# Kernel optimization log

Hardware: AMD Instinct MI355X
Metric: run time of the kernel (lower is better)

## Reference

```python
import jax, jax.numpy as jnp
import numpy as np

DIM = 1024
NUM_HEADS = 8
HEAD_DIM = 128
MAX_SEQ_LEN = 2048
ATTN_SCALE = 0.12
RMS_EPS = 1.1920929e-07  # torch float32 eps (F.rms_norm default)


def rms_norm(x):
    return x * jax.lax.rsqrt(jnp.mean(jnp.square(x), axis=-1, keepdims=True) + RMS_EPS)


def rope_tables(T):
    # angular_freq: (1/1024)**linspace(0,1,head_dim//4), padded with head_dim//4 zeros -> length head_dim//2
    af = (1.0 / 1024.0) ** np.linspace(0.0, 1.0, HEAD_DIM // 4, dtype=np.float32)
    af = np.concatenate([af, np.zeros(HEAD_DIM // 4, dtype=np.float32)])
    t = np.arange(T, dtype=np.float32)
    theta = np.einsum('i,j->ij', t, af)  # [T, head_dim//2]
    return jnp.asarray(np.cos(theta)), jnp.asarray(np.sin(theta))


def apply_rope(x_BTHD, cos, sin):
    # cos/sin: [T, head_dim//2] -> broadcast [1,T,1,hd//2]
    c = cos[None, :, None, :]
    s = sin[None, :, None, :]
    x1, x2 = jnp.split(x_BTHD, 2, axis=-1)
    y1 = x1 * c + x2 * s
    y2 = -x1 * s + x2 * c
    return jnp.concatenate([y1, y2], axis=-1)


def setup_inputs() -> dict:
    key = jax.random.key(0)
    k1, k2, k3, k4, k5 = jax.random.split(key, 5)
    B, T = 4, 2048
    hdim = NUM_HEADS * HEAD_DIM
    std = 0.5 * DIM ** (-0.5)
    bound = (3.0 ** 0.5) * std
    x = jax.random.normal(k1, (B, T, DIM), dtype=jnp.float32)
    ve = jax.random.normal(k2, (B, T, DIM), dtype=jnp.float32)
    sa_lambdas = jax.random.uniform(k3, (2,), dtype=jnp.float32)
    qkv_w = jax.random.uniform(k4, (3, hdim, DIM), dtype=jnp.float32, minval=-bound, maxval=bound)
    # original inits c_proj to zeros; use small random so the output is non-trivial
    c_proj_weight = jax.random.normal(k5, (DIM, hdim), dtype=jnp.float32) * 0.02
    return {"x": x, "ve": ve, "sa_lambdas": sa_lambdas, "qkv_w": qkv_w,
            "c_proj_weight": c_proj_weight}


def reference(x, ve, sa_lambdas, qkv_w, c_proj_weight):
    B, T, D = x.shape
    H, hd = NUM_HEADS, HEAD_DIM
    Wqkv = qkv_w.reshape(3 * H * hd, D)
    qkv = jnp.einsum('btd,ed->bte', x, Wqkv).reshape(B, T, 3 * H, hd)
    q, k, v = jnp.split(qkv, 3, axis=-2)  # each [B,T,H,hd]
    q, k = rms_norm(q), rms_norm(k)
    cos, sin = rope_tables(T)
    q, k = apply_rope(q, cos, sin), apply_rope(k, cos, sin)
    v = sa_lambdas[0] * v + sa_lambdas[1] * ve.reshape(B, T, H, hd)
    # [B,H,T,T] scores
    attn = jnp.einsum('bqhd,bkhd->bhqk', q, k) * ATTN_SCALE
    causal = jnp.triu(jnp.ones((T, T), dtype=bool), k=1)
    attn = jnp.where(causal[None, None], -jnp.inf, attn)
    attn = jax.nn.softmax(attn, axis=-1)
    y = jnp.einsum('bhqk,bkhd->bqhd', attn, v).reshape(B, T, H * hd)
    return jnp.einsum('bte,de->btd', y, c_proj_weight)
```

## Files before the change

kernel.cpp:

```cpp
#include <hip/hip_runtime.h>

#define DIM 1024
#define NH 8
#define HD 128
#define T_SEQ 2048
#define NTOK 8192
#define QKV_N 3072
#define ATTN_SCALE 0.12f
#define RMS_EPS 1.1920929e-07f

using f32x4  = __attribute__((ext_vector_type(4))) float;
using bf16x8 = __attribute__((ext_vector_type(8))) __bf16;

__device__ __forceinline__ unsigned short f2bf(float f) {
    unsigned int u = __builtin_bit_cast(unsigned int, f);
    u += 0x7fffu + ((u >> 16) & 1u);
    return (unsigned short)(u >> 16);
}
__device__ __forceinline__ float bf2f(unsigned short s) {
    unsigned int u = ((unsigned int)s) << 16;
    return __builtin_bit_cast(float, u);
}
__device__ __forceinline__ unsigned int cvtpk(float lo, float hi) {
    unsigned int r;
    asm("v_cvt_pk_bf16_f32 %0, %1, %2" : "=v"(r) : "v"(lo), "v"(hi));
    return r;
}

__device__ __forceinline__ void gll16(const void* g, void* l) {
    __builtin_amdgcn_global_load_lds(
        (const __attribute__((address_space(1))) unsigned int*)g,
        (__attribute__((address_space(3))) unsigned int*)l, 16, 0, 0);
}

#define VMCNT(n) asm volatile("s_waitcnt vmcnt(" #n ")" ::: "memory")

__global__ __launch_bounds__(256) void prep(const float* __restrict__ x,
                                            const float* __restrict__ qkvw,
                                            const float* __restrict__ cprojw,
                                            unsigned short* __restrict__ xb,
                                            unsigned short* __restrict__ wqb,
                                            unsigned short* __restrict__ cpb,
                                            float2* __restrict__ tab) {
    const int bid = blockIdx.x;
    const int tid = threadIdx.x;
    if (bid < 12288) {
        const float* in;
        unsigned short* out;
        int i;
        if (bid < 8192)        { in = x;      out = xb;  i = bid*256 + tid; }
        else if (bid < 11264)  { in = qkvw;   out = wqb; i = (bid-8192)*256 + tid; }
        else                   { in = cprojw; out = cpb; i = (bid-11264)*256 + tid; }
        float4 f = ((const float4*)in)[i];
        ushort4 o;
        o.x = f2bf(f.x); o.y = f2bf(f.y); o.z = f2bf(f.z); o.w = f2bf(f.w);
        ((ushort4*)out)[i] = o;
    } else {
        int idx = (bid - 12288)*256 + tid;
        int t = idx >> 5, i = idx & 31;
        float th = (float)t * exp2f((float)i * (-10.0f/31.0f));
        float sn, cs;
        sincosf(th, &sn, &cs);
        tab[idx] = make_float2(cs, sn);
    }
}

#define SLOT_A 32768
#define SLOT_SZ 49152

template<int OUTF32>
__global__ __launch_bounds__(512, 1) void gemm256(const unsigned short* __restrict__ A,
                                                  const unsigned short* __restrict__ B,
                                                  void* __restrict__ Cout,
                                                  int M, int N, int K, int nbn) {
    __shared__ __align__(16) char smem[147456];
    const int tid  = threadIdx.x;
    const int lane = tid & 63;
    const int w    = tid >> 6;
    const int wm   = w >> 1, wn = w & 1;
    const int lr   = lane & 15, lg = lane >> 4;
    const int xsw  = (lr & 7) << 3;

    const int chunk = gridDim.x >> 3;
    const int bid2  = (blockIdx.x & 7) * chunk + (blockIdx.x >> 3);
    const int m0 = (bid2 / nbn) * 256;
    const int n0 = (bid2 % nbn) * 128;

    const int rsub = lane >> 3;
    const int csw  = ((lane & 7) ^ rsub) << 3;

    char* s0 = smem;
    char* s1 = smem + SLOT_SZ;
    char* s2 = smem + 2*SLOT_SZ;

    auto stage = [&](int kt, char* slot) {
        const int kb = kt * 64;
        #pragma unroll
        for (int i = 0; i < 4; ++i) {
            int c = w*4 + i;
            gll16(&A[(size_t)(m0 + c*8 + rsub)*K + kb + csw], slot + c*1024);
        }
        #pragma unroll
        for (int i = 0; i < 2; ++i) {
            int c = w*2 + i;
            gll16(&B[(size_t)(n0 + c*8 + rsub)*K + kb + csw], slot + SLOT_A + c*1024);
        }
    };

    f32x4 acc[4][4] = {};
    const int KT = K / 64;

    stage(0, s0);
    stage(1, s1);
    VMCNT(6);
    __builtin_amdgcn_s_barrier();
    __builtin_amdgcn_sched_barrier(0);

    for (int t = 0; t < KT; ++t) {
        if (t + 2 < KT) stage(t + 2, s2);
        const unsigned short* sA = (const unsigned short*)s0;
        const unsigned short* sB = (const unsigned short*)(s0 + SLOT_A);
        bf16x8 bfr[4][2];
        #pragma unroll
        for (int n = 0; n < 4; ++n)
            #pragma unroll
            for (int kk = 0; kk < 2; ++kk)
                bfr[n][kk] = *(const bf16x8*)&sB[(wn*64 + n*16 + lr)*64 + ((kk*32 + lg*8) ^ xsw)];
        #pragma unroll
        for (int m = 0; m < 4; ++m) {
            bf16x8 af[2];
            #pragma unroll
            for (int kk = 0; kk < 2; ++kk)
                af[kk] = *(const bf16x8*)&sA[(wm*64 + m*16 + lr)*64 + ((kk*32 + lg*8) ^ xsw)];
            __builtin_amdgcn_s_setprio(1);
            #pragma unroll
            for (int n = 0; n < 4; ++n)
                #pragma unroll
                for (int kk = 0; kk < 2; ++kk)
                    acc[m][n] = __builtin_amdgcn_mfma_f32_16x16x32_bf16(af[kk], bfr[n][kk], acc[m][n], 0, 0, 0);
            __builtin_amdgcn_s_setprio(0);
        }
        if (t + 2 < KT) { VMCNT(6); }
        else            { VMCNT(0); }
        __builtin_amdgcn_s_barrier();
        __builtin_amdgcn_sched_barrier(0);
        char* tmp = s0; s0 = s1; s1 = s2; s2 = tmp;
    }

    __syncthreads();
    float* sc = (float*)(smem + (size_t)w * 17408);
    #pragma unroll
    for (int m = 0; m < 4; ++m)
        #pragma unroll
        for (int n = 0; n < 4; ++n)
            #pragma unroll
            for (int r = 0; r < 4; ++r)
                sc[(m*16 + lg*4 + r)*68 + n*16 + lr] = acc[m][n][r];

    if (OUTF32) {
        float* C = (float*)Cout;
        #pragma unroll
        for (int rnd = 0; rnd < 16; ++rnd) {
            int g = rnd*64 + lane;
            int row = g >> 4, c4 = (g & 15) * 4;
            float4 v = *(float4*)&sc[row*68 + c4];
            *(float4*)&C[(size_t)(m0 + wm*64 + row)*N + n0 + wn*64 + c4] = v;
        }
    } else {
        unsigned short* C = (unsigned short*)Cout;
        #pragma unroll
        for (int rnd = 0; rnd < 8; ++rnd) {
            int g = rnd*64 + lane;
            int row = g >> 3, c8 = (g & 7) * 8;
            float4 v0 = *(float4*)&sc[row*68 + c8];
            float4 v1 = *(float4*)&sc[row*68 + c8 + 4];
            uint4 o;
            o.x = f2bf(v0.x) | ((unsigned)f2bf(v0.y) << 16);
            o.y = f2bf(v0.z) | ((unsigned)f2bf(v0.w) << 16);
            o.z = f2bf(v1.x) | ((unsigned)f2bf(v1.y) << 16);
            o.w = f2bf(v1.z) | ((unsigned)f2bf(v1.w) << 16);
            *(uint4*)&C[(size_t)(m0 + wm*64 + row)*N + n0 + wn*64 + c8] = o;
        }
    }
}

__global__ __launch_bounds__(256) void qkv_post(const unsigned short* __restrict__ qkv,
                                                const float2* __restrict__ tab,
                                                unsigned short* __restrict__ qO,
                                                unsigned short* __restrict__ kO) {
    int gw   = (blockIdx.x * 256 + threadIdx.x) >> 6;
    int lane = threadIdx.x & 63;
    int h     = gw & 7;
    int token = gw >> 3;
    int t     = token & (T_SEQ-1);
    int b     = token >> 11;

    const unsigned short* base = qkv + (size_t)token * QKV_N + h*HD;
    float q1 = bf2f(base[lane]),        q2 = bf2f(base[lane+64]);
    float k1 = bf2f(base[1024+lane]),   k2 = bf2f(base[1024+lane+64]);

    float sq = q1*q1 + q2*q2;
    float sk = k1*k1 + k2*k2;
    #pragma unroll
    for (int m = 1; m < 64; m <<= 1) {
        sq += __shfl_xor(sq, m);
        sk += __shfl_xor(sk, m);
    }
    float qs = rsqrtf(sq * (1.0f/128.0f) + RMS_EPS) * (ATTN_SCALE * 1.44269504088896f);
    float ks = rsqrtf(sk * (1.0f/128.0f) + RMS_EPS);
    q1 *= qs; q2 *= qs; k1 *= ks; k2 *= ks;

    float cs = 1.0f, sn = 0.0f;
    if (lane < 32) { float2 cc = tab[t*32 + lane]; cs = cc.x; sn = cc.y; }
    float qy1 =  q1*cs + q2*sn, qy2 = -q1*sn + q2*cs;
    float ky1 =  k1*cs + k2*sn, ky2 = -k1*sn + k2*cs;

    size_t obase = ((size_t)(b*NH + h) * T_SEQ + t) * HD;
    qO[obase + lane]      = f2bf(qy1);
    qO[obase + lane + 64] = f2bf(qy2);
    kO[obase + lane]      = f2bf(ky1);
    kO[obase + lane + 64] = f2bf(ky2);
}

__global__ __launch_bounds__(256) void vmix_t(const unsigned short* __restrict__ qkv,
                                              const float* __restrict__ ve,
                                              const float* __restrict__ lam,
                                              unsigned short* __restrict__ vt) {
    __shared__ unsigned short lT[128*72];
    const int tid = threadIdx.x;
    const int t0  = blockIdx.x * 64;
    const int bh  = blockIdx.y;
    const int b = bh >> 3, h = bh & 7;
    const float l0 = lam[0], l1 = lam[1];

    #pragma unroll
    for (int it = 0; it < 4; ++it) {
        int g  = it*256 + tid;
        int t  = g >> 4;
        int d8 = (g & 15) << 3;
        size_t token = (size_t)b*T_SEQ + t0 + t;
        ushort4 v0 = *(const ushort4*)&qkv[token*QKV_N + 2048 + h*HD + d8];
        ushort4 v1 = *(const ushort4*)&qkv[token*QKV_N + 2048 + h*HD + d8 + 4];
        float4 e0 = *(const float4*)&ve[token*DIM + h*HD + d8];
        float4 e1 = *(const float4*)&ve[token*DIM + h*HD + d8 + 4];
        lT[(d8+0)*72 + t] = f2bf(l0*bf2f(v0.x) + l1*e0.x);
        lT[(d8+1)*72 + t] = f2bf(l0*bf2f(v0.y) + l1*e0.y);
        lT[(d8+2)*72 + t] = f2bf(l0*bf2f(v0.z) + l1*e0.z);
        lT[(d8+3)*72 + t] = f2bf(l0*bf2f(v0.w) + l1*e0.w);
        lT[(d8+4)*72 + t] = f2bf(l0*bf2f(v1.x) + l1*e1.x);
        lT[(d8+5)*72 + t] = f2bf(l0*bf2f(v1.y) + l1*e1.y);
        lT[(d8+6)*72 + t] = f2bf(l0*bf2f(v1.z) + l1*e1.z);
        lT[(d8+7)*72 + t] = f2bf(l0*bf2f(v1.w) + l1*e1.w);
    }
    __syncthreads();
    #pragma unroll
    for (int it = 0; it < 4; ++it) {
        int g  = it*256 + tid;
        int d  = g >> 3;
        int t8 = (g & 7) << 3;
        uint4 pk = *(const uint4*)&lT[d*72 + t8];
        *(uint4*)&vt[((size_t)bh*HD + d)*T_SEQ + t0 + t8] = pk;
    }
}

__global__ __launch_bounds__(256, 2) void attn_fwd(const unsigned short* __restrict__ Q,
                                                   const unsigned short* __restrict__ K,
                                                   const unsigned short* __restrict__ Vt,
                                                   unsigned short* __restrict__ Y) {
    __shared__ unsigned short lK[2][64*128];
    __shared__ unsigned short lV[2][128*64];
    __shared__ unsigned short lP[4][16*72];
    __shared__ float lden[4][2][16];

    const int tid  = threadIdx.x;
    const int lane = tid & 63;
    const int w    = tid >> 6;
    const int lr   = lane & 15, lg = lane >> 4;

    const int lin = blockIdx.y * 16 + blockIdx.x;
    const int bh  = (lin & 7)*4 + ((lin >> 3) & 3);
    const int p   = lin >> 5;
    const int qtA = p, qtB = 31 - p;

    const unsigned short* Qg = Q  + (size_t)bh * T_SEQ * HD;
    const unsigned short* Kg = K  + (size_t)bh * T_SEQ * HD;
    const unsigned short* Vg = Vt + (size_t)bh * HD * T_SEQ;
    const int q0A = qtA*64 + w*16;
    const int q0B = qtB*64 + w*16;

    auto stage = [&](int kt, int s) {
        const int kbase = kt * 64;
        #pragma unroll
        for (int i = 0; i < 4; ++i) {
            int c = w*4 + i;
            int row = c*4 + (lane >> 4);
            int col = ((lane & 15) << 3) ^ ((row & 7) << 3);
            gll16(&Kg[(size_t)(kbase + row)*HD + col], &lK[s][c*512]);
        }
        #pragma unroll
        for (int i = 0; i < 4; ++i) {
            int c = w*4 + i;
            int row = c*8 + (lane >> 3);
            int col = ((lane & 7) << 3) ^ ((row & 7) << 3);
            gll16(&Vg[(size_t)row*T_SEQ + kbase + col], &lV[s][c*512]);
        }
    };

    bf16x8 qfA[4], qfB[4];
    #pragma unroll
    for (int kk = 0; kk < 4; ++kk) {
        qfA[kk] = *(const bf16x8*)&Qg[(size_t)(q0A + lr)*HD + kk*32 + lg*8];
        qfB[kk] = *(const bf16x8*)&Qg[(size_t)(q0B + lr)*HD + kk*32 + lg*8];
    }
    VMCNT(0);
    #pragma unroll
    for (int kk = 0; kk < 4; ++kk)
        asm volatile("" :: "v"(qfA[kk]), "v"(qfB[kk]));

    f32x4 oA[8] = {}, oB[8] = {};
    float psA = 0.f, psB = 0.f;

    auto softmax_store = [&](f32x4* sf, float& ps) {
        #pragma unroll
        for (int j = 0; j < 4; ++j)
            #pragma unroll
            for (int r = 0; r < 4; ++r) {
                float pp = exp2f(sf[j][r]);
                sf[j][r] = pp;
                ps += pp;
            }
        #pragma unroll
        for (int j = 0; j < 4; ++j) {
            uint2 pk;
            pk.x = cvtpk(sf[j][0], sf[j][1]);
            pk.y = cvtpk(sf[j][2], sf[j][3]);
            *(uint2*)&lP[w][lr*72 + j*16 + lg*4] = pk;
        }
        asm volatile("" ::: "memory");
    };

    auto passAB = [&](bool diagA, int kbase,
                      const unsigned short* lKc, const unsigned short* lVc) {
        f32x4 sfA[4], sfB[4];
        __builtin_amdgcn_s_setprio(1);
        #pragma unroll
        for (int j = 0; j < 4; ++j) {
            f32x4 sA = {0.f,0.f,0.f,0.f}, sB = {0.f,0.f,0.f,0.f};
            #pragma unroll
            for (int kk = 0; kk < 4; ++kk) {
                bf16x8 kf = *(const bf16x8*)&lKc[(j*16+lr)*128 + ((kk*32 + lg*8) ^ ((lr&7)<<3))];
                sA = __builtin_amdgcn_mfma_f32_16x16x32_bf16(kf, qfA[kk], sA, 0, 0, 0);
                sB = __builtin_amdgcn_mfma_f32_16x16x32_bf16(kf, qfB[kk], sB, 0, 0, 0);
            }
            sfA[j] = sA; sfB[j] = sB;
        }
        __builtin_amdgcn_s_setprio(0);
        if (diagA) {
            #pragma unroll
            for (int j = 0; j < 4; ++j)
                #pragma unroll
                for (int r = 0; r < 4; ++r) {
                    int kcol = kbase + j*16 + lg*4 + r;
                    int qrow = q0A + lr;
                    if (kcol > qrow) sfA[j][r] = -INFINITY;
                }
        }
        softmax_store(sfA, psA);
        bf16x8 pfA[2];
        #pragma unroll
        for (int kk = 0; kk < 2; ++kk)
            pfA[kk] = *(const bf16x8*)&lP[w][lr*72 + kk*32 + lg*8];
        asm volatile("" ::: "memory");
        softmax_store(sfB, psB);
        bf16x8 pfB[2];
        #pragma unroll
        for (int kk = 0; kk < 2; ++kk)
            pfB[kk] = *(const bf16x8*)&lP[w][lr*72 + kk*32 + lg*8];
        #pragma unroll
        for (int n = 0; n < 8; ++n) {
            bf16x8 vf0 = *(const bf16x8*)&lVc[(n*16+lr)*64 + (( 0 + lg*8) ^ ((lr&7)<<3))];
            bf16x8 vf1 = *(const bf16x8*)&lVc[(n*16+lr)*64 + ((32 + lg*8) ^ ((lr&7)<<3))];
            __builtin_amdgcn_s_setprio(1);
            oA[n] = __builtin_amdgcn_mfma_f32_16x16x32_bf16(pfA[0], vf0, oA[n], 0, 0, 0);
            oB[n] = __builtin_amdgcn_mfma_f32_16x16x32_bf16(pfB[0], vf0, oB[n], 0, 0, 0);
            oA[n] = __builtin_amdgcn_mfma_f32_16x16x32_bf16(pfA[1], vf1, oA[n], 0, 0, 0);
            oB[n] = __builtin_amdgcn_mfma_f32_16x16x32_bf16(pfB[1], vf1, oB[n], 0, 0, 0);
            __builtin_amdgcn_s_setprio(0);
        }
    };

    auto pass = [&](bool diag, int kbase,
                    const unsigned short* lKc, const unsigned short* lVc) {
        f32x4 sf[4];
        __builtin_amdgcn_s_setprio(1);
        #pragma unroll
        for (int j = 0; j < 4; ++j) {
            f32x4 s = {0.f,0.f,0.f,0.f};
            #pragma unroll
            for (int kk = 0; kk < 4; ++kk) {
                bf16x8 kf = *(const bf16x8*)&lKc[(j*16+lr)*128 + ((kk*32 + lg*8) ^ ((lr&7)<<3))];
                s = __builtin_amdgcn_mfma_f32_16x16x32_bf16(kf, qfB[kk], s, 0, 0, 0);
            }
            sf[j] = s;
        }
        __builtin_amdgcn_s_setprio(0);
        if (diag) {
            #pragma unroll
            for (int j = 0; j < 4; ++j)
                #pragma unroll
                for (int r = 0; r < 4; ++r) {
                    int kcol = kbase + j*16 + lg*4 + r;
                    int qrow = q0B + lr;
                    if (kcol > qrow) sf[j][r] = -INFINITY;
                }
        }
        softmax_store(sf, psB);
        bf16x8 pf[2];
        #pragma unroll
        for (int kk = 0; kk < 2; ++kk)
            pf[kk] = *(const bf16x8*)&lP[w][lr*72 + kk*32 + lg*8];
        #pragma unroll
        for (int n = 0; n < 8; ++n) {
            bf16x8 vf0 = *(const bf16x8*)&lVc[(n*16+lr)*64 + (( 0 + lg*8) ^ ((lr&7)<<3))];
            bf16x8 vf1 = *(const bf16x8*)&lVc[(n*16+lr)*64 + ((32 + lg*8) ^ ((lr&7)<<3))];
            __builtin_amdgcn_s_setprio(1);
            oB[n] = __builtin_amdgcn_mfma_f32_16x16x32_bf16(pf[0], vf0, oB[n], 0, 0, 0);
            oB[n] = __builtin_amdgcn_mfma_f32_16x16x32_bf16(pf[1], vf1, oB[n], 0, 0, 0);
            __builtin_amdgcn_s_setprio(0);
        }
    };

    stage(0, 0);
    for (int kt = 0; kt <= qtB; ++kt) {
        __builtin_amdgcn_s_barrier();
        const bool pre = (kt + 1 <= qtB);
        if (pre) stage(kt + 1, (kt + 1) & 1);
        if (pre) { VMCNT(8); } else { VMCNT(0); }
        __builtin_amdgcn_sched_barrier(0);
        const int kbase = kt * 64;
        const unsigned short* lKc = lK[kt & 1];
        const unsigned short* lVc = lV[kt & 1];
        if (kt <= qtA) passAB(kt == qtA, kbase, lKc, lVc);
        else           pass(kt == qtB, kbase, lKc, lVc);
    }

    psA += __shfl_xor(psA, 16); psA += __shfl_xor(psA, 32);
    psB += __shfl_xor(psB, 16); psB += __shfl_xor(psB, 32);
    if (lane < 16) { lden[w][0][lane] = psA; lden[w][1][lane] = psB; }
    asm volatile("" ::: "memory");
    float riA[4], riB[4];
    #pragma unroll
    for (int r = 0; r < 4; ++r) {
        riA[r] = 1.0f / lden[w][0][lg*4 + r];
        riB[r] = 1.0f / lden[w][1][lg*4 + r];
    }

    const int b = bh >> 3, h = bh & 7;
    #pragma unroll
    for (int n = 0; n < 8; ++n)
        #pragma unroll
        for (int r = 0; r < 4; ++r) {
            int d = n*16 + lr;
            int qrowA = q0A + lg*4 + r;
            int qrowB = q0B + lg*4 + r;
            Y[((size_t)(b*T_SEQ + qrowA))*DIM + h*HD + d] = f2bf(oA[n][r] * riA[r]);
            Y[((size_t)(b*T_SEQ + qrowB))*DIM + h*HD + d] = f2bf(oB[n][r] * riB[r]);
        }
}

extern "C" void kernel_launch(void* const* d_in, const int* in_sizes, int n_in,
                              void* d_out, int out_size, void* d_ws, size_t ws_size,
                              hipStream_t stream) {
    const float* x      = (const float*)d_in[0];
    const float* ve     = (const float*)d_in[1];
    const float* lam    = (const float*)d_in[2];
    const float* qkvw   = (const float*)d_in[3];
    const float* cprojw = (const float*)d_in[4];

    char* ws = (char*)d_ws;
    unsigned short* xb  = (unsigned short*)(ws);
    unsigned short* wqb = (unsigned short*)(ws + 16777216);
    unsigned short* cpb = (unsigned short*)(ws + 23068672);
    unsigned short* qkv = (unsigned short*)(ws + 25165824);
    unsigned short* qa  = (unsigned short*)(ws + 75497472);
    unsigned short* ka  = (unsigned short*)(ws + 92274688);
    unsigned short* vt  = (unsigned short*)(ws + 109051904);
    unsigned short* ya  = (unsigned short*)(ws + 125829120);
    float2* tab = (float2*)(ws + 142606336);

    prep<<<12544, 256, 0, stream>>>(x, qkvw, cprojw, xb, wqb, cpb, tab);

    gemm256<0><<<768, 512, 0, stream>>>(xb, wqb, qkv, NTOK, QKV_N, DIM, 24);
    qkv_post<<<16384, 256, 0, stream>>>(qkv, tab, qa, ka);
    vmix_t<<<dim3(32, 32), 256, 0, stream>>>(qkv, ve, lam, vt);
    attn_fwd<<<dim3(16, 32), 256, 0, stream>>>(qa, ka, vt, ya);
    gemm256<1><<<256, 512, 0, stream>>>(ya, cpb, (float*)d_out, NTOK, DIM, DIM, 8);
}
```

Baseline: 195.4 us.

## Fuse QKV epilogue: RMSNorm, RoPE, V mix and transpose into GEMM

Adds a specialized QKV GEMM kernel whose epilogue stages the 256x128 tile in LDS and applies RMSNorm, scaling and RoPE for Q/K heads, or the lambda mix with ve plus a transposed write for V heads. This removes the intermediate bf16 qkv buffer round-trip and two separate kernel launches. It also stops rounding qkv to bf16 before normalization. The attention kernel's softmax is split into pack and store phases so the second tile's exponentials can overlap the first tile's P store and load. The fused epilogue is serial per warp, 32 rows per wave, so it may lengthen the GEMM tail.

```diff
diff --git a/kernel.cpp b/kernel.cpp
--- a/kernel.cpp
+++ b/kernel.cpp
@@ -68,6 +68,152 @@
 #define SLOT_A 32768
 #define SLOT_SZ 49152
 
+__global__ __launch_bounds__(512, 1) void gemm_qkv(const unsigned short* __restrict__ A,
+                                                   const unsigned short* __restrict__ B,
+                                                   const float* __restrict__ ve,
+                                                   const float* __restrict__ lam,
+                                                   const float2* __restrict__ tab,
+                                                   unsigned short* __restrict__ qa,
+                                                   unsigned short* __restrict__ ka,
+                                                   unsigned short* __restrict__ vt,
+                                                   int M, int N, int K, int nbn) {
+    __shared__ __align__(16) char smem[147456];
+    const int tid  = threadIdx.x;
+    const int lane = tid & 63;
+    const int w    = tid >> 6;
+    const int wm   = w >> 1, wn = w & 1;
+    const int lr   = lane & 15, lg = lane >> 4;
+    const int xsw  = (lr & 7) << 3;
+
+    const int chunk = gridDim.x >> 3;
+    const int bid2  = (blockIdx.x & 7) * chunk + (blockIdx.x >> 3);
+    const int m0 = (bid2 / nbn) * 256;
+    const int n0 = (bid2 % nbn) * 128;
+
+    const int rsub = lane >> 3;
+    const int csw  = ((lane & 7) ^ rsub) << 3;
+
+    char* s0 = smem;
+    char* s1 = smem + SLOT_SZ;
+    char* s2 = smem + 2*SLOT_SZ;
+
+    auto stage = [&](int kt, char* slot) {
+        const int kb = kt * 64;
+        #pragma unroll
+        for (int i = 0; i < 4; ++i) {
+            int c = w*4 + i;
+            gll16(&A[(size_t)(m0 + c*8 + rsub)*K + kb + csw], slot + c*1024);
+        }
+        #pragma unroll
+        for (int i = 0; i < 2; ++i) {
+            int c = w*2 + i;
+            gll16(&B[(size_t)(n0 + c*8 + rsub)*K + kb + csw], slot + SLOT_A + c*1024);
+        }
+    };
+
+    f32x4 acc[4][4] = {};
+    const int KT = K / 64;
+
+    stage(0, s0);
+    stage(1, s1);
+    VMCNT(6);
+    __builtin_amdgcn_s_barrier();
+    __builtin_amdgcn_sched_barrier(0);
+
+    for (int t = 0; t < KT; ++t) {
+        if (t + 2 < KT) stage(t + 2, s2);
+        const unsigned short* sA = (const unsigned short*)s0;
+        const unsigned short* sB = (const unsigned short*)(s0 + SLOT_A);
+        bf16x8 bfr[4][2];
+        #pragma unroll
+        for (int n = 0; n < 4; ++n)
+            #pragma unroll
+            for (int kk = 0; kk < 2; ++kk)
+                bfr[n][kk] = *(const bf16x8*)&sB[(wn*64 + n*16 + lr)*64 + ((kk*32 + lg*8) ^ xsw)];
+        #pragma unroll
+        for (int m = 0; m < 4; ++m) {
+            bf16x8 af[2];
+            #pragma unroll
+            for (int kk = 0; kk < 2; ++kk)
+                af[kk] = *(const bf16x8*)&sA[(wm*64 + m*16 + lr)*64 + ((kk*32 + lg*8) ^ xsw)];
+            __builtin_amdgcn_s_setprio(1);
+            #pragma unroll
+            for (int n = 0; n < 4; ++n)
+                #pragma unroll
+                for (int kk = 0; kk < 2; ++kk)
+                    acc[m][n] = __builtin_amdgcn_mfma_f32_16x16x32_bf16(af[kk], bfr[n][kk], acc[m][n], 0, 0, 0);
+            __builtin_amdgcn_s_setprio(0);
+        }
+        if (t + 2 < KT) { VMCNT(6); }
+        else            { VMCNT(0); }
+        __builtin_amdgcn_s_barrier();
+        __builtin_amdgcn_sched_barrier(0);
+        char* tmp = s0; s0 = s1; s1 = s2; s2 = tmp;
+    }
+
+    __syncthreads();
+    float* C = (float*)smem;
+    #pragma unroll
+    for (int m = 0; m < 4; ++m)
+        #pragma unroll
+        for (int n = 0; n < 4; ++n)
+            #pragma unroll
+            for (int r = 0; r < 4; ++r)
+                C[(wm*64 + m*16 + lg*4 + r)*133 + wn*64 + n*16 + lr] = acc[m][n][r];
+    __syncthreads();
+
+    const int htyp = n0 >> 7;
+    if (htyp < 16) {
+        const bool isQ = (htyp < 8);
+        const int h = htyp & 7;
+        unsigned short* out = isQ ? qa : ka;
+        const float smul = isQ ? (ATTN_SCALE * 1.44269504088896f) : 1.0f;
+        for (int rr = 0; rr < 32; ++rr) {
+            int row = w*32 + rr;
+            int token = m0 + row;
+            int t = token & (T_SEQ-1), b = token >> 11;
+            float v1 = C[row*133 + lane];
+            float v2 = C[row*133 + lane + 64];
+            float s = v1*v1 + v2*v2;
+            #pragma unroll
+            for (int mm = 1; mm < 64; mm <<= 1) s += __shfl_xor(s, mm);
+            float sc2 = rsqrtf(s * (1.0f/128.0f) + RMS_EPS) * smul;
+            v1 *= sc2; v2 *= sc2;
+            float cs = 1.0f, sn = 0.0f;
+            if (lane < 32) { float2 cc = tab[t*32 + lane]; cs = cc.x; sn = cc.y; }
+            float y1 =  v1*cs + v2*sn;
+            float y2 = -v1*sn + v2*cs;
+            size_t ob = ((size_t)(b*NH + h) * T_SEQ + t) * HD;
+            out[ob + lane]      = f2bf(y1);
+            out[ob + lane + 64] = f2bf(y2);
+        }
+    } else {
+        const int h = htyp - 16;
+        const float l0 = lam[0], l1 = lam[1];
+        for (int rr = 0; rr < 32; ++rr) {
+            int row = w*32 + rr;
+            size_t token = (size_t)(m0 + row);
+            float e1 = ve[token*DIM + h*HD + lane];
+            float e2 = ve[token*DIM + h*HD + lane + 64];
+            C[row*133 + lane]      = l0 * C[row*133 + lane]      + l1*e1;
+            C[row*133 + lane + 64] = l0 * C[row*133 + lane + 64] + l1*e2;
+        }
+        __syncthreads();
+        const int b = m0 >> 11, t0 = m0 & (T_SEQ-1);
+        for (int dd = 0; dd < 16; ++dd) {
+            int d = w*16 + dd;
+            float x0 = C[(lane*4+0)*133 + d];
+            float x1 = C[(lane*4+1)*133 + d];
+            float x2 = C[(lane*4+2)*133 + d];
+            float x3 = C[(lane*4+3)*133 + d];
+            uint2 o;
+            o.x = f2bf(x0) | ((unsigned)f2bf(x1) << 16);
+            o.y = f2bf(x2) | ((unsigned)f2bf(x3) << 16);
+            *(uint2*)&vt[((size_t)(b*NH + h) * HD + d) * T_SEQ + t0 + lane*4] = o;
+        }
+    }
+}
+
 template<int OUTF32>
 __global__ __launch_bounds__(512, 1) void gemm256(const unsigned short* __restrict__ A,
                                                   const unsigned short* __restrict__ B,
@@ -158,16 +304,16 @@
                 sc[(m*16 + lg*4 + r)*68 + n*16 + lr] = acc[m][n][r];
 
     if (OUTF32) {
-        float* C = (float*)Cout;
+        float* Cg = (float*)Cout;
         #pragma unroll
         for (int rnd = 0; rnd < 16; ++rnd) {
             int g = rnd*64 + lane;
             int row = g >> 4, c4 = (g & 15) * 4;
             float4 v = *(float4*)&sc[row*68 + c4];
-            *(float4*)&C[(size_t)(m0 + wm*64 + row)*N + n0 + wn*64 + c4] = v;
+            *(float4*)&Cg[(size_t)(m0 + wm*64 + row)*N + n0 + wn*64 + c4] = v;
         }
     } else {
-        unsigned short* C = (unsigned short*)Cout;
+        unsigned short* Cg = (unsigned short*)Cout;
         #pragma unroll
         for (int rnd = 0; rnd < 8; ++rnd) {
             int g = rnd*64 + lane;
@@ -179,87 +325,8 @@
             o.y = f2bf(v0.z) | ((unsigned)f2bf(v0.w) << 16);
             o.z = f2bf(v1.x) | ((unsigned)f2bf(v1.y) << 16);
             o.w = f2bf(v1.z) | ((unsigned)f2bf(v1.w) << 16);
-            *(uint4*)&C[(size_t)(m0 + wm*64 + row)*N + n0 + wn*64 + c8] = o;
-        }
-    }
-}
-
-__global__ __launch_bounds__(256) void qkv_post(const unsigned short* __restrict__ qkv,
-                                                const float2* __restrict__ tab,
-                                                unsigned short* __restrict__ qO,
-                                                unsigned short* __restrict__ kO) {
-    int gw   = (blockIdx.x * 256 + threadIdx.x) >> 6;
-    int lane = threadIdx.x & 63;
-    int h     = gw & 7;
-    int token = gw >> 3;
-    int t     = token & (T_SEQ-1);
-    int b     = token >> 11;
-
-    const unsigned short* base = qkv + (size_t)token * QKV_N + h*HD;
-    float q1 = bf2f(base[lane]),        q2 = bf2f(base[lane+64]);
-    float k1 = bf2f(base[1024+lane]),   k2 = bf2f(base[1024+lane+64]);
-
-    float sq = q1*q1 + q2*q2;
-    float sk = k1*k1 + k2*k2;
-    #pragma unroll
-    for (int m = 1; m < 64; m <<= 1) {
-        sq += __shfl_xor(sq, m);
-        sk += __shfl_xor(sk, m);
-    }
-    float qs = rsqrtf(sq * (1.0f/128.0f) + RMS_EPS) * (ATTN_SCALE * 1.44269504088896f);
-    float ks = rsqrtf(sk * (1.0f/128.0f) + RMS_EPS);
-    q1 *= qs; q2 *= qs; k1 *= ks; k2 *= ks;
-
-    float cs = 1.0f, sn = 0.0f;
-    if (lane < 32) { float2 cc = tab[t*32 + lane]; cs = cc.x; sn = cc.y; }
-    float qy1 =  q1*cs + q2*sn, qy2 = -q1*sn + q2*cs;
-    float ky1 =  k1*cs + k2*sn, ky2 = -k1*sn + k2*cs;
-
-    size_t obase = ((size_t)(b*NH + h) * T_SEQ + t) * HD;
-    qO[obase + lane]      = f2bf(qy1);
-    qO[obase + lane + 64] = f2bf(qy2);
-    kO[obase + lane]      = f2bf(ky1);
-    kO[obase + lane + 64] = f2bf(ky2);
-}
-
-__global__ __launch_bounds__(256) void vmix_t(const unsigned short* __restrict__ qkv,
-                                              const float* __restrict__ ve,
-                                              const float* __restrict__ lam,
-                                              unsigned short* __restrict__ vt) {
-    __shared__ unsigned short lT[128*72];
-    const int tid = threadIdx.x;
-    const int t0  = blockIdx.x * 64;
-    const int bh  = blockIdx.y;
-    const int b = bh >> 3, h = bh & 7;
-    const float l0 = lam[0], l1 = lam[1];
-
-    #pragma unroll
-    for (int it = 0; it < 4; ++it) {
-        int g  = it*256 + tid;
-        int t  = g >> 4;
-        int d8 = (g & 15) << 3;
-        size_t token = (size_t)b*T_SEQ + t0 + t;
-        ushort4 v0 = *(const ushort4*)&qkv[token*QKV_N + 2048 + h*HD + d8];
-        ushort4 v1 = *(const ushort4*)&qkv[token*QKV_N + 2048 + h*HD + d8 + 4];
-        float4 e0 = *(const float4*)&ve[token*DIM + h*HD + d8];
-        float4 e1 = *(const float4*)&ve[token*DIM + h*HD + d8 + 4];
-        lT[(d8+0)*72 + t] = f2bf(l0*bf2f(v0.x) + l1*e0.x);
-        lT[(d8+1)*72 + t] = f2bf(l0*bf2f(v0.y) + l1*e0.y);
-        lT[(d8+2)*72 + t] = f2bf(l0*bf2f(v0.z) + l1*e0.z);
-        lT[(d8+3)*72 + t] = f2bf(l0*bf2f(v0.w) + l1*e0.w);
-        lT[(d8+4)*72 + t] = f2bf(l0*bf2f(v1.x) + l1*e1.x);
-        lT[(d8+5)*72 + t] = f2bf(l0*bf2f(v1.y) + l1*e1.y);
-        lT[(d8+6)*72 + t] = f2bf(l0*bf2f(v1.z) + l1*e1.z);
-        lT[(d8+7)*72 + t] = f2bf(l0*bf2f(v1.w) + l1*e1.w);
-    }
-    __syncthreads();
-    #pragma unroll
-    for (int it = 0; it < 4; ++it) {
-        int g  = it*256 + tid;
-        int d  = g >> 3;
-        int t8 = (g & 7) << 3;
-        uint4 pk = *(const uint4*)&lT[d*72 + t8];
-        *(uint4*)&vt[((size_t)bh*HD + d)*T_SEQ + t0 + t8] = pk;
+            *(uint4*)&Cg[(size_t)(m0 + wm*64 + row)*N + n0 + wn*64 + c8] = o;
+        }
     }
 }
 
@@ -320,7 +387,7 @@
     f32x4 oA[8] = {}, oB[8] = {};
     float psA = 0.f, psB = 0.f;
 
-    auto softmax_store = [&](f32x4* sf, float& ps) {
+    auto softmax_pack = [&](f32x4* sf, float& ps, uint2* pk) {
         #pragma unroll
         for (int j = 0; j < 4; ++j)
             #pragma unroll
@@ -331,11 +398,14 @@
             }
         #pragma unroll
         for (int j = 0; j < 4; ++j) {
-            uint2 pk;
-            pk.x = cvtpk(sf[j][0], sf[j][1]);
-            pk.y = cvtpk(sf[j][2], sf[j][3]);
-            *(uint2*)&lP[w][lr*72 + j*16 + lg*4] = pk;
-        }
+            pk[j].x = cvtpk(sf[j][0], sf[j][1]);
+            pk[j].y = cvtpk(sf[j][2], sf[j][3]);
+        }
+    };
+    auto p_store = [&](uint2* pk) {
+        #pragma unroll
+        for (int j = 0; j < 4; ++j)
+            *(uint2*)&lP[w][lr*72 + j*16 + lg*4] = pk[j];
         asm volatile("" ::: "memory");
     };
 
@@ -365,13 +435,16 @@
                     if (kcol > qrow) sfA[j][r] = -INFINITY;
                 }
         }
-        softmax_store(sfA, psA);
+        uint2 pkA[4], pkB[4];
+        softmax_pack(sfA, psA, pkA);
+        p_store(pkA);
+        softmax_pack(sfB, psB, pkB);
         bf16x8 pfA[2];
         #pragma unroll
         for (int kk = 0; kk < 2; ++kk)
             pfA[kk] = *(const bf16x8*)&lP[w][lr*72 + kk*32 + lg*8];
         asm volatile("" ::: "memory");
-        softmax_store(sfB, psB);
+        p_store(pkB);
         bf16x8 pfB[2];
         #pragma unroll
         for (int kk = 0; kk < 2; ++kk)
@@ -414,7 +487,9 @@
                     if (kcol > qrow) sf[j][r] = -INFINITY;
                 }
         }
-        softmax_store(sf, psB);
+        uint2 pk[4];
+        softmax_pack(sf, psB, pk);
+        p_store(pk);
         bf16x8 pf[2];
         #pragma unroll
         for (int kk = 0; kk < 2; ++kk)
@@ -481,7 +556,6 @@
     unsigned short* xb  = (unsigned short*)(ws);
     unsigned short* wqb = (unsigned short*)(ws + 16777216);
     unsigned short* cpb = (unsigned short*)(ws + 23068672);
-    unsigned short* qkv = (unsigned short*)(ws + 25165824);
     unsigned short* qa  = (unsigned short*)(ws + 75497472);
     unsigned short* ka  = (unsigned short*)(ws + 92274688);
     unsigned short* vt  = (unsigned short*)(ws + 109051904);
@@ -490,9 +564,8 @@
 
     prep<<<12544, 256, 0, stream>>>(x, qkvw, cprojw, xb, wqb, cpb, tab);
 
-    gemm256<0><<<768, 512, 0, stream>>>(xb, wqb, qkv, NTOK, QKV_N, DIM, 24);
-    qkv_post<<<16384, 256, 0, stream>>>(qkv, tab, qa, ka);
-    vmix_t<<<dim3(32, 32), 256, 0, stream>>>(qkv, ve, lam, vt);
+    gemm_qkv<<<768, 512, 0, stream>>>(xb, wqb, ve, lam, tab, qa, ka, vt,
+                                      NTOK, QKV_N, DIM, 24);
     attn_fwd<<<dim3(16, 32), 256, 0, stream>>>(qa, ka, vt, ya);
     gemm256<1><<<256, 512, 0, stream>>>(ya, cpb, (float*)d_out, NTOK, DIM, DIM, 8);
 }
```

Result: slower. 199.6 us (+2.1%).

## Fuse Q norm/rope into attention load and merge post kernels

Applied to the files above, without the earlier changes.

The Q RMS-norm and RoPE step moves into the attention kernel's Q-fragment load, which now reads Q straight from the qkv buffer. This removes the separate Q write and read round-trip through global memory. The K post-processing and the V mix/transpose kernels are merged into one launch, which cuts launch count. The softmax P packing is split from its LDS store so the B tile's exp/pack can be interleaved before the A tile's P read.

```diff
diff --git a/kernel.cpp b/kernel.cpp
--- a/kernel.cpp
+++ b/kernel.cpp
@@ -158,16 +158,16 @@
                 sc[(m*16 + lg*4 + r)*68 + n*16 + lr] = acc[m][n][r];
 
     if (OUTF32) {
-        float* C = (float*)Cout;
+        float* Cg = (float*)Cout;
         #pragma unroll
         for (int rnd = 0; rnd < 16; ++rnd) {
             int g = rnd*64 + lane;
             int row = g >> 4, c4 = (g & 15) * 4;
             float4 v = *(float4*)&sc[row*68 + c4];
-            *(float4*)&C[(size_t)(m0 + wm*64 + row)*N + n0 + wn*64 + c4] = v;
+            *(float4*)&Cg[(size_t)(m0 + wm*64 + row)*N + n0 + wn*64 + c4] = v;
         }
     } else {
-        unsigned short* C = (unsigned short*)Cout;
+        unsigned short* Cg = (unsigned short*)Cout;
         #pragma unroll
         for (int rnd = 0; rnd < 8; ++rnd) {
             int g = rnd*64 + lane;
@@ -179,93 +179,81 @@
             o.y = f2bf(v0.z) | ((unsigned)f2bf(v0.w) << 16);
             o.z = f2bf(v1.x) | ((unsigned)f2bf(v1.y) << 16);
             o.w = f2bf(v1.z) | ((unsigned)f2bf(v1.w) << 16);
-            *(uint4*)&C[(size_t)(m0 + wm*64 + row)*N + n0 + wn*64 + c8] = o;
+            *(uint4*)&Cg[(size_t)(m0 + wm*64 + row)*N + n0 + wn*64 + c8] = o;
         }
     }
 }
 
-__global__ __launch_bounds__(256) void qkv_post(const unsigned short* __restrict__ qkv,
-                                                const float2* __restrict__ tab,
-                                                unsigned short* __restrict__ qO,
-                                                unsigned short* __restrict__ kO) {
-    int gw   = (blockIdx.x * 256 + threadIdx.x) >> 6;
-    int lane = threadIdx.x & 63;
-    int h     = gw & 7;
-    int token = gw >> 3;
-    int t     = token & (T_SEQ-1);
-    int b     = token >> 11;
-
-    const unsigned short* base = qkv + (size_t)token * QKV_N + h*HD;
-    float q1 = bf2f(base[lane]),        q2 = bf2f(base[lane+64]);
-    float k1 = bf2f(base[1024+lane]),   k2 = bf2f(base[1024+lane+64]);
-
-    float sq = q1*q1 + q2*q2;
-    float sk = k1*k1 + k2*k2;
-    #pragma unroll
-    for (int m = 1; m < 64; m <<= 1) {
-        sq += __shfl_xor(sq, m);
-        sk += __shfl_xor(sk, m);
+__global__ __launch_bounds__(256) void post(const unsigned short* __restrict__ qkv,
+                                            const float* __restrict__ ve,
+                                            const float* __restrict__ lam,
+                                            const float2* __restrict__ tab,
+                                            unsigned short* __restrict__ kO,
+                                            unsigned short* __restrict__ vt) {
+    __shared__ unsigned short lT[128*72];
+    const int bid = blockIdx.x;
+    const int tid = threadIdx.x;
+    if (bid < 16384) {
+        int gw   = (bid*256 + tid) >> 6;
+        int lane = tid & 63;
+        int h     = gw & 7;
+        int token = gw >> 3;
+        int t     = token & (T_SEQ-1);
+        int b     = token >> 11;
+        const unsigned short* base = qkv + (size_t)token * QKV_N + 1024 + h*HD;
+        float k1 = bf2f(base[lane]), k2 = bf2f(base[lane+64]);
+        float sk = k1*k1 + k2*k2;
+        #pragma unroll
+        for (int m = 1; m < 64; m <<= 1) sk += __shfl_xor(sk, m);
+        float ks = rsqrtf(sk * (1.0f/128.0f) + RMS_EPS);
+        k1 *= ks; k2 *= ks;
+        float cs = 1.0f, sn = 0.0f;
+        if (lane < 32) { float2 cc = tab[t*32 + lane]; cs = cc.x; sn = cc.y; }
+        float ky1 =  k1*cs + k2*sn, ky2 = -k1*sn + k2*cs;
+        size_t obase = ((size_t)(b*NH + h) * T_SEQ + t) * HD;
+        kO[obase + lane]      = f2bf(ky1);
+        kO[obase + lane + 64] = f2bf(ky2);
+    } else {
+        const int idx = bid - 16384;
+        const int t0  = (idx & 31) * 64;
+        const int bh  = idx >> 5;
+        const int b = bh >> 3, h = bh & 7;
+        const float l0 = lam[0], l1 = lam[1];
+        #pragma unroll
+        for (int it = 0; it < 4; ++it) {
+            int g  = it*256 + tid;
+            int t  = g >> 4;
+            int d8 = (g & 15) << 3;
+            size_t token = (size_t)b*T_SEQ + t0 + t;
+            ushort4 v0 = *(const ushort4*)&qkv[token*QKV_N + 2048 + h*HD + d8];
+            ushort4 v1 = *(const ushort4*)&qkv[token*QKV_N + 2048 + h*HD + d8 + 4];
+            float4 e0 = *(const float4*)&ve[token*DIM + h*HD + d8];
+            float4 e1 = *(const float4*)&ve[token*DIM + h*HD + d8 + 4];
+            lT[(d8+0)*72 + t] = f2bf(l0*bf2f(v0.x) + l1*e0.x);
+            lT[(d8+1)*72 + t] = f2bf(l0*bf2f(v0.y) + l1*e0.y);
+            lT[(d8+2)*72 + t] = f2bf(l0*bf2f(v0.z) + l1*e0.z);
+            lT[(d8+3)*72 + t] = f2bf(l0*bf2f(v0.w) + l1*e0.w);
+            lT[(d8+4)*72 + t] = f2bf(l0*bf2f(v1.x) + l1*e1.x);
+            lT[(d8+5)*72 + t] = f2bf(l0*bf2f(v1.y) + l1*e1.y);
+            lT[(d8+6)*72 + t] = f2bf(l0*bf2f(v1.z) + l1*e1.z);
+            lT[(d8+7)*72 + t] = f2bf(l0*bf2f(v1.w) + l1*e1.w);
+        }
+        __syncthreads();
+        #pragma unroll
+        for (int it = 0; it < 4; ++it) {
+            int g  = it*256 + tid;
+            int d  = g >> 3;
+            int t8 = (g & 7) << 3;
+            uint4 pk = *(const uint4*)&lT[d*72 + t8];
+            *(uint4*)&vt[((size_t)bh*HD + d)*T_SEQ + t0 + t8] = pk;
+        }
     }
-    float qs = rsqrtf(sq * (1.0f/128.0f) + RMS_EPS) * (ATTN_SCALE * 1.44269504088896f);
-    float ks = rsqrtf(sk * (1.0f/128.0f) + RMS_EPS);
-    q1 *= qs; q2 *= qs; k1 *= ks; k2 *= ks;
-
-    float cs = 1.0f, sn = 0.0f;
-    if (lane < 32) { float2 cc = tab[t*32 + lane]; cs = cc.x; sn = cc.y; }
-    float qy1 =  q1*cs + q2*sn, qy2 = -q1*sn + q2*cs;
-    float ky1 =  k1*cs + k2*sn, ky2 = -k1*sn + k2*cs;
-
-    size_t obase = ((size_t)(b*NH + h) * T_SEQ + t) * HD;
-    qO[obase + lane]      = f2bf(qy1);
-    qO[obase + lane + 64] = f2bf(qy2);
-    kO[obase + lane]      = f2bf(ky1);
-    kO[obase + lane + 64] = f2bf(ky2);
-}
-
-__global__ __launch_bounds__(256) void vmix_t(const unsigned short* __restrict__ qkv,
-                                              const float* __restrict__ ve,
-                                              const float* __restrict__ lam,
-                                              unsigned short* __restrict__ vt) {
-    __shared__ unsigned short lT[128*72];
-    const int tid = threadIdx.x;
-    const int t0  = blockIdx.x * 64;
-    const int bh  = blockIdx.y;
-    const int b = bh >> 3, h = bh & 7;
-    const float l0 = lam[0], l1 = lam[1];
-
-    #pragma unroll
-    for (int it = 0; it < 4; ++it) {
-        int g  = it*256 + tid;
-        int t  = g >> 4;
-        int d8 = (g & 15) << 3;
-        size_t token = (size_t)b*T_SEQ + t0 + t;
-        ushort4 v0 = *(const ushort4*)&qkv[token*QKV_N + 2048 + h*HD + d8];
-        ushort4 v1 = *(const ushort4*)&qkv[token*QKV_N + 2048 + h*HD + d8 + 4];
-        float4 e0 = *(const float4*)&ve[token*DIM + h*HD + d8];
-        float4 e1 = *(const float4*)&ve[token*DIM + h*HD + d8 + 4];
-        lT[(d8+0)*72 + t] = f2bf(l0*bf2f(v0.x) + l1*e0.x);
-        lT[(d8+1)*72 + t] = f2bf(l0*bf2f(v0.y) + l1*e0.y);
-        lT[(d8+2)*72 + t] = f2bf(l0*bf2f(v0.z) + l1*e0.z);
-        lT[(d8+3)*72 + t] = f2bf(l0*bf2f(v0.w) + l1*e0.w);
-        lT[(d8+4)*72 + t] = f2bf(l0*bf2f(v1.x) + l1*e1.x);
-        lT[(d8+5)*72 + t] = f2bf(l0*bf2f(v1.y) + l1*e1.y);
-        lT[(d8+6)*72 + t] = f2bf(l0*bf2f(v1.z) + l1*e1.z);
-        lT[(d8+7)*72 + t] = f2bf(l0*bf2f(v1.w) + l1*e1.w);
-    }
-    __syncthreads();
-    #pragma unroll
-    for (int it = 0; it < 4; ++it) {
-        int g  = it*256 + tid;
-        int d  = g >> 3;
-        int t8 = (g & 7) << 3;
-        uint4 pk = *(const uint4*)&lT[d*72 + t8];
-        *(uint4*)&vt[((size_t)bh*HD + d)*T_SEQ + t0 + t8] = pk;
-    }
-}
-
-__global__ __launch_bounds__(256, 2) void attn_fwd(const unsigned short* __restrict__ Q,
+}
+
+__global__ __launch_bounds__(256, 2) void attn_fwd(const unsigned short* __restrict__ qkv,
                                                    const unsigned short* __restrict__ K,
                                                    const unsigned short* __restrict__ Vt,
+                                                   const float2* __restrict__ tab,
                                                    unsigned short* __restrict__ Y) {
     __shared__ unsigned short lK[2][64*128];
     __shared__ unsigned short lV[2][128*64];
@@ -281,8 +269,8 @@
     const int bh  = (lin & 7)*4 + ((lin >> 3) & 3);
     const int p   = lin >> 5;
     const int qtA = p, qtB = 31 - p;
-
-    const unsigned short* Qg = Q  + (size_t)bh * T_SEQ * HD;
+    const int b = bh >> 3, h = bh & 7;
+
     const unsigned short* Kg = K  + (size_t)bh * T_SEQ * HD;
     const unsigned short* Vg = Vt + (size_t)bh * HD * T_SEQ;
     const int q0A = qtA*64 + w*16;
@@ -306,12 +294,46 @@
         }
     };
 
+    auto loadQ = [&](int q0, bf16x8* qf) {
+        const unsigned short* qg = qkv + ((size_t)(b*T_SEQ + q0 + lr))*QKV_N + h*HD;
+        float v[4][8];
+        #pragma unroll
+        for (int kk = 0; kk < 4; ++kk) {
+            ushort4 u0 = *(const ushort4*)&qg[kk*32 + lg*8];
+            ushort4 u1 = *(const ushort4*)&qg[kk*32 + lg*8 + 4];
+            v[kk][0]=bf2f(u0.x); v[kk][1]=bf2f(u0.y); v[kk][2]=bf2f(u0.z); v[kk][3]=bf2f(u0.w);
+            v[kk][4]=bf2f(u1.x); v[kk][5]=bf2f(u1.y); v[kk][6]=bf2f(u1.z); v[kk][7]=bf2f(u1.w);
+        }
+        float s = 0.f;
+        #pragma unroll
+        for (int kk = 0; kk < 4; ++kk)
+            #pragma unroll
+            for (int e = 0; e < 8; ++e) s += v[kk][e]*v[kk][e];
+        s += __shfl_xor(s, 16); s += __shfl_xor(s, 32);
+        float sc = rsqrtf(s * (1.0f/128.0f) + RMS_EPS) * (ATTN_SCALE * 1.44269504088896f);
+        float y[4][8];
+        #pragma unroll
+        for (int e = 0; e < 8; ++e) {
+            float2 cc = tab[(q0 + lr)*32 + lg*8 + e];
+            y[0][e] = ( v[0][e]*cc.x + v[2][e]*cc.y) * sc;
+            y[2][e] = (-v[0][e]*cc.y + v[2][e]*cc.x) * sc;
+            y[1][e] = v[1][e] * sc;
+            y[3][e] = v[3][e] * sc;
+        }
+        #pragma unroll
+        for (int kk = 0; kk < 4; ++kk) {
+            uint4 pk;
+            pk.x = cvtpk(y[kk][0], y[kk][1]);
+            pk.y = cvtpk(y[kk][2], y[kk][3]);
+            pk.z = cvtpk(y[kk][4], y[kk][5]);
+            pk.w = cvtpk(y[kk][6], y[kk][7]);
+            qf[kk] = __builtin_bit_cast(bf16x8, pk);
+        }
+    };
+
     bf16x8 qfA[4], qfB[4];
-    #pragma unroll
-    for (int kk = 0; kk < 4; ++kk) {
-        qfA[kk] = *(const bf16x8*)&Qg[(size_t)(q0A + lr)*HD + kk*32 + lg*8];
-        qfB[kk] = *(const bf16x8*)&Qg[(size_t)(q0B + lr)*HD + kk*32 + lg*8];
-    }
+    loadQ(q0A, qfA);
+    loadQ(q0B, qfB);
     VMCNT(0);
     #pragma unroll
     for (int kk = 0; kk < 4; ++kk)
@@ -320,7 +342,7 @@
     f32x4 oA[8] = {}, oB[8] = {};
     float psA = 0.f, psB = 0.f;
 
-    auto softmax_store = [&](f32x4* sf, float& ps) {
+    auto softmax_pack = [&](f32x4* sf, float& ps, uint2* pk) {
         #pragma unroll
         for (int j = 0; j < 4; ++j)
             #pragma unroll
@@ -331,11 +353,14 @@
             }
         #pragma unroll
         for (int j = 0; j < 4; ++j) {
-            uint2 pk;
-            pk.x = cvtpk(sf[j][0], sf[j][1]);
-            pk.y = cvtpk(sf[j][2], sf[j][3]);
-            *(uint2*)&lP[w][lr*72 + j*16 + lg*4] = pk;
-        }
+            pk[j].x = cvtpk(sf[j][0], sf[j][1]);
+            pk[j].y = cvtpk(sf[j][2], sf[j][3]);
+        }
+    };
+    auto p_store = [&](uint2* pk) {
+        #pragma unroll
+        for (int j = 0; j < 4; ++j)
+            *(uint2*)&lP[w][lr*72 + j*16 + lg*4] = pk[j];
         asm volatile("" ::: "memory");
     };
 
@@ -365,13 +390,16 @@
                     if (kcol > qrow) sfA[j][r] = -INFINITY;
                 }
         }
-        softmax_store(sfA, psA);
+        uint2 pkA[4], pkB[4];
+        softmax_pack(sfA, psA, pkA);
+        p_store(pkA);
+        softmax_pack(sfB, psB, pkB);
         bf16x8 pfA[2];
         #pragma unroll
         for (int kk = 0; kk < 2; ++kk)
             pfA[kk] = *(const bf16x8*)&lP[w][lr*72 + kk*32 + lg*8];
         asm volatile("" ::: "memory");
-        softmax_store(sfB, psB);
+        p_store(pkB);
         bf16x8 pfB[2];
         #pragma unroll
         for (int kk = 0; kk < 2; ++kk)
@@ -414,7 +442,9 @@
                     if (kcol > qrow) sf[j][r] = -INFINITY;
                 }
         }
-        softmax_store(sf, psB);
+        uint2 pk[4];
+        softmax_pack(sf, psB, pk);
+        p_store(pk);
         bf16x8 pf[2];
         #pragma unroll
         for (int kk = 0; kk < 2; ++kk)
@@ -455,7 +485,6 @@
         riB[r] = 1.0f / lden[w][1][lg*4 + r];
     }
 
-    const int b = bh >> 3, h = bh & 7;
     #pragma unroll
     for (int n = 0; n < 8; ++n)
         #pragma unroll
@@ -482,7 +511,6 @@
     unsigned short* wqb = (unsigned short*)(ws + 16777216);
     unsigned short* cpb = (unsigned short*)(ws + 23068672);
     unsigned short* qkv = (unsigned short*)(ws + 25165824);
-    unsigned short* qa  = (unsigned short*)(ws + 75497472);
     unsigned short* ka  = (unsigned short*)(ws + 92274688);
     unsigned short* vt  = (unsigned short*)(ws + 109051904);
     unsigned short* ya  = (unsigned short*)(ws + 125829120);
@@ -491,8 +519,7 @@
     prep<<<12544, 256, 0, stream>>>(x, qkvw, cprojw, xb, wqb, cpb, tab);
 
     gemm256<0><<<768, 512, 0, stream>>>(xb, wqb, qkv, NTOK, QKV_N, DIM, 24);
-    qkv_post<<<16384, 256, 0, stream>>>(qkv, tab, qa, ka);
-    vmix_t<<<dim3(32, 32), 256, 0, stream>>>(qkv, ve, lam, vt);
-    attn_fwd<<<dim3(16, 32), 256, 0, stream>>>(qa, ka, vt, ya);
+    post<<<17408, 256, 0, stream>>>(qkv, ve, lam, tab, ka, vt);
+    attn_fwd<<<dim3(16, 32), 256, 0, stream>>>(qkv, ka, vt, tab, ya);
     gemm256<1><<<256, 512, 0, stream>>>(ya, cpb, (float*)d_out, NTOK, DIM, DIM, 8);
 }
```

New measurement: 197.1 us. About the same (+0.9%).
